# Kernel optimization log

Hardware: AMD Instinct MI355X
Metric: run time of the kernel (lower is better)

Reference implementation:

```python
import jax, jax.numpy as jnp
import numpy as np

H = 4096          # hidden_size (Llama-3.1-8B)
BLK = 32          # sca_block_size
NB = H // BLK     # 128 blocks
R = 4             # sca_block_rank
K = 3             # sca_top_k
SIGMA = 1.0       # sca_sigma
NUM_TASKS = 10


def setup_inputs() -> dict:
    key = jax.random.key(0)
    ks = jax.random.split(key, 9)
    B, S = 4, 4096
    x = jax.random.normal(ks[0], (B, S, H), jnp.float32)
    task_ids = jax.random.randint(ks[1], (B,), 0, NUM_TASKS)
    task_emb = jax.random.normal(ks[2], (NUM_TASKS, H), jnp.float32) * 0.02
    Wp = jax.random.normal(ks[3], (H, 3), jnp.float32) * (1.0 / np.sqrt(H))  # spatial_proj (xavier-ish)
    bp = jnp.zeros((3,), jnp.float32)
    centers = jax.random.normal(ks[4], (NB, 3), jnp.float32)                 # block_centers
    A = jax.random.normal(ks[5], (NB, H, R), jnp.float32) * 0.02             # per-block down proj
    Bm = jax.random.normal(ks[6], (NB, R, BLK), jnp.float32) * 0.02          # per-block up proj into its hidden slice
    adapter_scale = jnp.float32(1.0)
    return dict(x=x, task_ids=task_ids, task_emb=task_emb, Wp=Wp, bp=bp,
                centers=centers, A=A, Bm=Bm, adapter_scale=adapter_scale)


def reference(x, task_ids, task_emb, Wp, bp, centers, A, Bm, adapter_scale):
    # task conditioning
    h = x + task_emb[task_ids][:, None, :]                     # [B,S,H]
    # spatial routing: project tokens to 3D, Gaussian score vs block centers
    coords = h @ Wp + bp                                       # [B,S,3]
    d2 = jnp.sum((coords[:, :, None, :] - centers[None, None]) ** 2, axis=-1)  # [B,S,NB]
    scores = -d2 / (2.0 * SIGMA ** 2)
    top_s, top_i = jax.lax.top_k(scores, K)                    # [B,S,K]
    gates = jax.nn.softmax(top_s, axis=-1)                     # soft mask over selected blocks
    # low-rank adapter per block (dense spmm_impl): down-project against all blocks, gather top-k
    z = jnp.einsum('bsh,nhr->bsnr', h, A)                      # [B,S,NB,R]
    z_sel = jnp.take_along_axis(z, top_i[..., None], axis=2)   # [B,S,K,R]
    B_sel = Bm[top_i]                                          # [B,S,K,R,BLK]
    delta_blk = jnp.einsum('bskr,bskrc->bskc', z_sel, B_sel) * gates[..., None]  # [B,S,K,BLK]
    # scatter block outputs into their hidden slices
    Bn, Sn = x.shape[0], x.shape[1]
    cols = top_i[..., None] * BLK + jnp.arange(BLK)            # [B,S,K,BLK]
    bi = jnp.arange(Bn)[:, None, None, None]
    si = jnp.arange(Sn)[None, :, None, None]
    delta = jnp.zeros_like(x).at[bi, si, cols].add(delta_blk)  # [B,S,H]
    return x + adapter_scale * delta
```

## Files before the change

kernel.cpp:

```cpp
#include <hip/hip_runtime.h>
#include <math.h>

#define HDIM 4096
#define NBLK 128
#define RNK  4
#define TOPK 3

typedef float f4 __attribute__((ext_vector_type(4)));
typedef float f2 __attribute__((ext_vector_type(2)));
typedef unsigned int u32;
typedef u32 u4 __attribute__((ext_vector_type(4)));

__device__ __forceinline__ u32 pk_fp8(f4 v) {
    u32 w = (u32)__builtin_amdgcn_cvt_pk_fp8_f32(v.x, v.y, 0, false);
    w = (u32)__builtin_amdgcn_cvt_pk_fp8_f32(v.z, v.w, (int)w, true);
    return w;
}
__device__ __forceinline__ f2 upk_fp8(u32 w, bool hi) {
    typedef float vf2 __attribute__((ext_vector_type(2)));
    vf2 r = hi ? __builtin_amdgcn_cvt_pk_f32_fp8((int)w, true)
               : __builtin_amdgcn_cvt_pk_f32_fp8((int)w, false);
    f2 o; o.x = r.x; o.y = r.y; return o;
}

__global__ __launch_bounds__(256) void convert_A8(
    const float* __restrict__ A, u32* __restrict__ Af8)
{
    int d = blockIdx.x * 256 + threadIdx.x;
    const f4* src = reinterpret_cast<const f4*>(A) + 4 * (size_t)d;
    f4 r0 = __builtin_nontemporal_load(src + 0);
    f4 r1 = __builtin_nontemporal_load(src + 1);
    f4 r2 = __builtin_nontemporal_load(src + 2);
    f4 r3 = __builtin_nontemporal_load(src + 3);
    u4 o;
    o.x = pk_fp8(r0); o.y = pk_fp8(r1); o.z = pk_fp8(r2); o.w = pk_fp8(r3);
    reinterpret_cast<u4*>(Af8)[d] = o;
}

__global__ __launch_bounds__(256) void npl_fused(
    const float* __restrict__ x,
    const int*   __restrict__ task_ids,
    const float* __restrict__ task_emb,
    const float* __restrict__ Wp,
    const float* __restrict__ bp,
    const float* __restrict__ centers,
    const u32*   __restrict__ Af8,
    const float* __restrict__ Bm,
    const float* __restrict__ scale_p,
    float* __restrict__ out,
    int S_per_batch)
{
    __shared__ float h_lds[HDIM];
    __shared__ float redc[4][4];
    __shared__ float redz[4][12];

    const int tid  = threadIdx.x;
    const int wid  = tid >> 6;
    const int lane = tid & 63;
    const int token = blockIdx.x;
    const int b = token / S_per_batch;
    const int task = task_ids[b];

    const float* xrow = x + (size_t)token * HDIM;
    const float* trow = task_emb + (size_t)task * HDIM;
    float*       orow = out + (size_t)token * HDIM;

    const f4* xr4 = reinterpret_cast<const f4*>(xrow);
    const f4* tr4 = reinterpret_cast<const f4*>(trow);
    f4*       or4 = reinterpret_cast<f4*>(orow);

    f4 xv[4];
    float c0 = 0.f, c1 = 0.f, c2 = 0.f;
#pragma unroll
    for (int k = 0; k < 4; ++k) {
        int i4 = tid + k * 256;
        f4 xx = __builtin_nontemporal_load(xr4 + i4);
        f4 tt = tr4[i4];
        xv[k] = xx;
        f4 hh = xx + tt;
        reinterpret_cast<f4*>(h_lds)[i4] = hh;
        int e = i4 * 4;
        const float* wrow = Wp + (size_t)e * 3;
        c0 += hh.x * wrow[0];  c1 += hh.x * wrow[1];  c2 += hh.x * wrow[2];
        c0 += hh.y * wrow[3];  c1 += hh.y * wrow[4];  c2 += hh.y * wrow[5];
        c0 += hh.z * wrow[6];  c1 += hh.z * wrow[7];  c2 += hh.z * wrow[8];
        c0 += hh.w * wrow[9];  c1 += hh.w * wrow[10]; c2 += hh.w * wrow[11];
    }
#pragma unroll
    for (int off = 32; off; off >>= 1) {
        c0 += __shfl_down(c0, off);
        c1 += __shfl_down(c1, off);
        c2 += __shfl_down(c2, off);
    }
    if (lane == 0) { redc[wid][0] = c0; redc[wid][1] = c1; redc[wid][2] = c2; }
    __syncthreads();

    c0 = redc[0][0] + redc[1][0] + redc[2][0] + redc[3][0] + bp[0];
    c1 = redc[0][1] + redc[1][1] + redc[2][1] + redc[3][1] + bp[1];
    c2 = redc[0][2] + redc[1][2] + redc[2][2] + redc[3][2] + bp[2];

    float dx = c0 - centers[lane * 3 + 0];
    float dy = c1 - centers[lane * 3 + 1];
    float dz = c2 - centers[lane * 3 + 2];
    float v1 = -0.5f * (dx * dx + dy * dy + dz * dz);
    dx = c0 - centers[(lane + 64) * 3 + 0];
    dy = c1 - centers[(lane + 64) * 3 + 1];
    dz = c2 - centers[(lane + 64) * 3 + 2];
    float v2 = -0.5f * (dx * dx + dy * dy + dz * dz);

    float tv0, tv1, tv2; int n0, n1, n2;
#pragma unroll
    for (int kk = 0; kk < TOPK; ++kk) {
        float v = v1; int idx = lane;
        if (v2 > v || (v2 == v && (lane + 64) < idx)) { v = v2; idx = lane + 64; }
#pragma unroll
        for (int off = 32; off; off >>= 1) {
            float ov = __shfl_down(v, off);
            int   oi = __shfl_down(idx, off);
            if (ov > v || (ov == v && oi < idx)) { v = ov; idx = oi; }
        }
        idx = __shfl(idx, 0);
        v   = __shfl(v, 0);
        if (kk == 0)      { tv0 = v; n0 = idx; }
        else if (kk == 1) { tv1 = v; n1 = idx; }
        else              { tv2 = v; n2 = idx; }
        if (idx == lane)      v1 = -3.0e38f;
        if (idx == lane + 64) v2 = -3.0e38f;
    }

    float m  = tv0;
    float e0 = 1.0f;
    float e1 = expf(tv1 - m);
    float e2 = expf(tv2 - m);
    float inv = 1.0f / (e0 + e1 + e2);
    float s = scale_p[0];
    float g0 = e0 * inv * s;
    float g1 = e1 * inv * s;
    float g2 = e2 * inv * s;

    float zp[TOPK][RNK];
#pragma unroll
    for (int kk = 0; kk < TOPK; ++kk)
#pragma unroll
        for (int r = 0; r < RNK; ++r) zp[kk][r] = 0.f;

#pragma unroll
    for (int kk = 0; kk < TOPK; ++kk) {
        int n = (kk == 0) ? n0 : (kk == 1) ? n1 : n2;
        const u4* Ab = reinterpret_cast<const u4*>(Af8) + (size_t)n * 1024;
#pragma unroll
        for (int k = 0; k < 4; ++k) {
            int idx = tid + k * 256;
            u4 q = Ab[idx];
            f4 hv = reinterpret_cast<const f4*>(h_lds)[idx];
            f2 p;
            p = upk_fp8(q.x, false); zp[kk][0] += hv.x * p.x; zp[kk][1] += hv.x * p.y;
            p = upk_fp8(q.x, true);  zp[kk][2] += hv.x * p.x; zp[kk][3] += hv.x * p.y;
            p = upk_fp8(q.y, false); zp[kk][0] += hv.y * p.x; zp[kk][1] += hv.y * p.y;
            p = upk_fp8(q.y, true);  zp[kk][2] += hv.y * p.x; zp[kk][3] += hv.y * p.y;
            p = upk_fp8(q.z, false); zp[kk][0] += hv.z * p.x; zp[kk][1] += hv.z * p.y;
            p = upk_fp8(q.z, true);  zp[kk][2] += hv.z * p.x; zp[kk][3] += hv.z * p.y;
            p = upk_fp8(q.w, false); zp[kk][0] += hv.w * p.x; zp[kk][1] += hv.w * p.y;
            p = upk_fp8(q.w, true);  zp[kk][2] += hv.w * p.x; zp[kk][3] += hv.w * p.y;
        }
    }
#pragma unroll
    for (int off = 32; off; off >>= 1) {
#pragma unroll
        for (int kk = 0; kk < TOPK; ++kk)
#pragma unroll
            for (int r = 0; r < RNK; ++r)
                zp[kk][r] += __shfl_down(zp[kk][r], off);
    }
    if (lane == 0) {
#pragma unroll
        for (int kk = 0; kk < TOPK; ++kk)
#pragma unroll
            for (int r = 0; r < RNK; ++r)
                redz[wid][kk * RNK + r] = zp[kk][r];
    }
    __syncthreads();

    float zf_[12];
#pragma unroll
    for (int t = 0; t < 12; ++t)
        zf_[t] = redz[0][t] + redz[1][t] + redz[2][t] + redz[3][t];

#pragma unroll
    for (int k = 0; k < 4; ++k) {
        int i4 = tid + k * 256;
        int e = i4 * 4;
        int bb = e >> 5;
        f4 o = xv[k];
        int kk = (bb == n0) ? 0 : (bb == n1) ? 1 : (bb == n2) ? 2 : -1;
        if (kk >= 0) {
            int nn = (kk == 0) ? n0 : (kk == 1) ? n1 : n2;
            float za = (kk == 0) ? zf_[0] : (kk == 1) ? zf_[4] : zf_[8];
            float zb = (kk == 0) ? zf_[1] : (kk == 1) ? zf_[5] : zf_[9];
            float zc = (kk == 0) ? zf_[2] : (kk == 1) ? zf_[6] : zf_[10];
            float zd = (kk == 0) ? zf_[3] : (kk == 1) ? zf_[7] : zf_[11];
            float gg = (kk == 0) ? g0 : (kk == 1) ? g1 : g2;
            const float* bm = Bm + (size_t)nn * 128;
            int c = e & 31;
            float d0 = za * bm[c + 0] + zb * bm[32 + c + 0] + zc * bm[64 + c + 0] + zd * bm[96 + c + 0];
            float d1 = za * bm[c + 1] + zb * bm[32 + c + 1] + zc * bm[64 + c + 1] + zd * bm[96 + c + 1];
            float d2 = za * bm[c + 2] + zb * bm[32 + c + 2] + zc * bm[64 + c + 2] + zd * bm[96 + c + 2];
            float d3 = za * bm[c + 3] + zb * bm[32 + c + 3] + zc * bm[64 + c + 3] + zd * bm[96 + c + 3];
            o.x += d0 * gg;
            o.y += d1 * gg;
            o.z += d2 * gg;
            o.w += d3 * gg;
        }
        __builtin_nontemporal_store(o, or4 + i4);
    }
}

extern "C" void kernel_launch(void* const* d_in, const int* in_sizes, int n_in,
                              void* d_out, int out_size, void* d_ws, size_t ws_size,
                              hipStream_t stream) {
    const float* x        = (const float*)d_in[0];
    const int*   task_ids = (const int*)  d_in[1];
    const float* task_emb = (const float*)d_in[2];
    const float* Wp       = (const float*)d_in[3];
    const float* bp       = (const float*)d_in[4];
    const float* centers  = (const float*)d_in[5];
    const float* A        = (const float*)d_in[6];
    const float* Bm       = (const float*)d_in[7];
    const float* scale    = (const float*)d_in[8];

    int tokens = in_sizes[0] / HDIM;
    int B      = in_sizes[1];
    int S      = tokens / B;

    u32* Af8 = (u32*)d_ws;

    const int n_u4 = NBLK * HDIM * RNK / 16;
    convert_A8<<<dim3(n_u4 / 256), dim3(256), 0, stream>>>(A, Af8);
    npl_fused<<<dim3(tokens), dim3(256), 0, stream>>>(
        x, task_ids, task_emb, Wp, bp, centers, Af8, Bm, scale,
        (float*)d_out, S);
}
```

Measured before the change: 196.4 us.

## Single-pass top-3 wave merge, interleave A loads, drop cached x registers

Replaces the three serial argmax wave reductions with one butterfly pass that merges sorted top-3 lists across lanes. The fp8 A-row loads for the three selected blocks are interleaved so all three are in flight at once. x is no longer kept in registers; the output rebuilds it as h minus the task embedding reread from LDS and global memory. This lowers register pressure and latency at the cost of extra reads, and the subtraction may not reproduce x exactly in floating point.

```diff
diff --git a/kernel.cpp b/kernel.cpp
--- a/kernel.cpp
+++ b/kernel.cpp
@@ -69,14 +69,12 @@
     const f4* tr4 = reinterpret_cast<const f4*>(trow);
     f4*       or4 = reinterpret_cast<f4*>(orow);
 
-    f4 xv[4];
     float c0 = 0.f, c1 = 0.f, c2 = 0.f;
 #pragma unroll
     for (int k = 0; k < 4; ++k) {
         int i4 = tid + k * 256;
         f4 xx = __builtin_nontemporal_load(xr4 + i4);
         f4 tt = tr4[i4];
-        xv[k] = xx;
         f4 hh = xx + tt;
         reinterpret_cast<f4*>(h_lds)[i4] = hh;
         int e = i4 * 4;
@@ -108,25 +106,34 @@
     dz = c2 - centers[(lane + 64) * 3 + 2];
     float v2 = -0.5f * (dx * dx + dy * dy + dz * dz);
 
-    float tv0, tv1, tv2; int n0, n1, n2;
-#pragma unroll
-    for (int kk = 0; kk < TOPK; ++kk) {
-        float v = v1; int idx = lane;
-        if (v2 > v || (v2 == v && (lane + 64) < idx)) { v = v2; idx = lane + 64; }
-#pragma unroll
-        for (int off = 32; off; off >>= 1) {
-            float ov = __shfl_down(v, off);
-            int   oi = __shfl_down(idx, off);
-            if (ov > v || (ov == v && oi < idx)) { v = ov; idx = oi; }
-        }
-        idx = __shfl(idx, 0);
-        v   = __shfl(v, 0);
-        if (kk == 0)      { tv0 = v; n0 = idx; }
-        else if (kk == 1) { tv1 = v; n1 = idx; }
-        else              { tv2 = v; n2 = idx; }
-        if (idx == lane)      v1 = -3.0e38f;
-        if (idx == lane + 64) v2 = -3.0e38f;
-    }
+    float av, bv, cv; int ai, bi, ci;
+    {
+        bool f = (v1 > v2) || (v1 == v2);
+        av = f ? v1 : v2;  ai = f ? lane : (lane + 64);
+        bv = f ? v2 : v1;  bi = f ? (lane + 64) : lane;
+        cv = -3.0e38f;     ci = 0x7fffffff;
+    }
+#pragma unroll
+    for (int off = 1; off < 64; off <<= 1) {
+        float oav = __shfl_xor(av, off); int oai = __shfl_xor(ai, off);
+        float obv = __shfl_xor(bv, off); int obi = __shfl_xor(bi, off);
+        float ocv = __shfl_xor(cv, off); int oci = __shfl_xor(ci, off);
+        bool t0 = (av > oav) || (av == oav && ai < oai);
+        float r0v = t0 ? av : oav;  int r0i = t0 ? ai : oai;
+        float lhv = t0 ? bv : av;   int lhi = t0 ? bi : ai;
+        float lnv = t0 ? cv : bv;   int lni = t0 ? ci : bi;
+        float mhv = t0 ? oav : obv; int mhi = t0 ? oai : obi;
+        float mnv = t0 ? obv : ocv; int mni = t0 ? obi : oci;
+        bool t1 = (lhv > mhv) || (lhv == mhv && lhi < mhi);
+        float r1v = t1 ? lhv : mhv; int r1i = t1 ? lhi : mhi;
+        float l2v = t1 ? lnv : lhv; int l2i = t1 ? lni : lhi;
+        float m2v = t1 ? mhv : mnv; int m2i = t1 ? mhi : mni;
+        bool t2 = (l2v > m2v) || (l2v == m2v && l2i < m2i);
+        float r2v = t2 ? l2v : m2v; int r2i = t2 ? l2i : m2i;
+        av = r0v; ai = r0i; bv = r1v; bi = r1i; cv = r2v; ci = r2i;
+    }
+    float tv0 = av, tv1 = bv, tv2 = cv;
+    int   n0  = ai, n1  = bi, n2  = ci;
 
     float m  = tv0;
     float e0 = 1.0f;
@@ -144,24 +151,44 @@
 #pragma unroll
         for (int r = 0; r < RNK; ++r) zp[kk][r] = 0.f;
 
-#pragma unroll
-    for (int kk = 0; kk < TOPK; ++kk) {
-        int n = (kk == 0) ? n0 : (kk == 1) ? n1 : n2;
-        const u4* Ab = reinterpret_cast<const u4*>(Af8) + (size_t)n * 1024;
+    {
+        const u4* A0 = reinterpret_cast<const u4*>(Af8) + (size_t)n0 * 1024;
+        const u4* A1 = reinterpret_cast<const u4*>(Af8) + (size_t)n1 * 1024;
+        const u4* A2 = reinterpret_cast<const u4*>(Af8) + (size_t)n2 * 1024;
 #pragma unroll
         for (int k = 0; k < 4; ++k) {
             int idx = tid + k * 256;
-            u4 q = Ab[idx];
+            u4 q0 = A0[idx];
+            u4 q1 = A1[idx];
+            u4 q2 = A2[idx];
             f4 hv = reinterpret_cast<const f4*>(h_lds)[idx];
             f2 p;
-            p = upk_fp8(q.x, false); zp[kk][0] += hv.x * p.x; zp[kk][1] += hv.x * p.y;
-            p = upk_fp8(q.x, true);  zp[kk][2] += hv.x * p.x; zp[kk][3] += hv.x * p.y;
-            p = upk_fp8(q.y, false); zp[kk][0] += hv.y * p.x; zp[kk][1] += hv.y * p.y;
-            p = upk_fp8(q.y, true);  zp[kk][2] += hv.y * p.x; zp[kk][3] += hv.y * p.y;
-            p = upk_fp8(q.z, false); zp[kk][0] += hv.z * p.x; zp[kk][1] += hv.z * p.y;
-            p = upk_fp8(q.z, true);  zp[kk][2] += hv.z * p.x; zp[kk][3] += hv.z * p.y;
-            p = upk_fp8(q.w, false); zp[kk][0] += hv.w * p.x; zp[kk][1] += hv.w * p.y;
-            p = upk_fp8(q.w, true);  zp[kk][2] += hv.w * p.x; zp[kk][3] += hv.w * p.y;
+            p = upk_fp8(q0.x, false); zp[0][0] += hv.x * p.x; zp[0][1] += hv.x * p.y;
+            p = upk_fp8(q0.x, true);  zp[0][2] += hv.x * p.x; zp[0][3] += hv.x * p.y;
+            p = upk_fp8(q0.y, false); zp[0][0] += hv.y * p.x; zp[0][1] += hv.y * p.y;
+            p = upk_fp8(q0.y, true);  zp[0][2] += hv.y * p.x; zp[0][3] += hv.y * p.y;
+            p = upk_fp8(q0.z, false); zp[0][0] += hv.z * p.x; zp[0][1] += hv.z * p.y;
+            p = upk_fp8(q0.z, true);  zp[0][2] += hv.z * p.x; zp[0][3] += hv.z * p.y;
+            p = upk_fp8(q0.w, false); zp[0][0] += hv.w * p.x; zp[0][1] += hv.w * p.y;
+            p = upk_fp8(q0.w, true);  zp[0][2] += hv.w * p.x; zp[0][3] += hv.w * p.y;
+
+            p = upk_fp8(q1.x, false); zp[1][0] += hv.x * p.x; zp[1][1] += hv.x * p.y;
+            p = upk_fp8(q1.x, true);  zp[1][2] += hv.x * p.x; zp[1][3] += hv.x * p.y;
+            p = upk_fp8(q1.y, false); zp[1][0] += hv.y * p.x; zp[1][1] += hv.y * p.y;
+            p = upk_fp8(q1.y, true);  zp[1][2] += hv.y * p.x; zp[1][3] += hv.y * p.y;
+            p = upk_fp8(q1.z, false); zp[1][0] += hv.z * p.x; zp[1][1] += hv.z * p.y;
+            p = upk_fp8(q1.z, true);  zp[1][2] += hv.z * p.x; zp[1][3] += hv.z * p.y;
+            p = upk_fp8(q1.w, false); zp[1][0] += hv.w * p.x; zp[1][1] += hv.w * p.y;
+            p = upk_fp8(q1.w, true);  zp[1][2] += hv.w * p.x; zp[1][3] += hv.w * p.y;
+
+            p = upk_fp8(q2.x, false); zp[2][0] += hv.x * p.x; zp[2][1] += hv.x * p.y;
+            p = upk_fp8(q2.x, true);  zp[2][2] += hv.x * p.x; zp[2][3] += hv.x * p.y;
+            p = upk_fp8(q2.y, false); zp[2][0] += hv.y * p.x; zp[2][1] += hv.y * p.y;
+            p = upk_fp8(q2.y, true);  zp[2][2] += hv.y * p.x; zp[2][3] += hv.y * p.y;
+            p = upk_fp8(q2.z, false); zp[2][0] += hv.z * p.x; zp[2][1] += hv.z * p.y;
+            p = upk_fp8(q2.z, true);  zp[2][2] += hv.z * p.x; zp[2][3] += hv.z * p.y;
+            p = upk_fp8(q2.w, false); zp[2][0] += hv.w * p.x; zp[2][1] += hv.w * p.y;
+            p = upk_fp8(q2.w, true);  zp[2][2] += hv.w * p.x; zp[2][3] += hv.w * p.y;
         }
     }
 #pragma unroll
@@ -191,7 +218,9 @@
         int i4 = tid + k * 256;
         int e = i4 * 4;
         int bb = e >> 5;
-        f4 o = xv[k];
+        f4 hh = reinterpret_cast<const f4*>(h_lds)[i4];
+        f4 tt = tr4[i4];
+        f4 o = hh - tt;
         int kk = (bb == n0) ? 0 : (bb == n1) ? 1 : (bb == n2) ? 2 : -1;
         if (kk >= 0) {
             int nn = (kk == 0) ? n0 : (kk == 1) ? n1 : n2;
```

New measurement: 204.0 us. 3.9% more time.

## Process two tokens per block with fp16 LDS and a single-pass top-3 merge

Applied to the files above, without the earlier changes.

Each 256-thread block now handles two tokens, launching half as many blocks. The task-conditioned hidden row is stored in LDS as packed fp16 instead of fp32, so both rows fit. The output residual is rebuilt as h minus task_emb rather than keeping x in registers. The three sequential top-1 reductions are replaced by one butterfly merge of per-lane top-3 lists, and the three A-block loads are interleaved. The aim is to cut barriers, register pressure and routing latency per token and to keep more memory traffic in flight. The cost is fp16 rounding error on the residual x path and on h in the down-projection, plus the extra task_emb reread.

```diff
diff --git a/kernel.cpp b/kernel.cpp
--- a/kernel.cpp
+++ b/kernel.cpp
@@ -8,6 +8,7 @@
 
 typedef float f4 __attribute__((ext_vector_type(4)));
 typedef float f2 __attribute__((ext_vector_type(2)));
+typedef _Float16 h2 __attribute__((ext_vector_type(2)));
 typedef unsigned int u32;
 typedef u32 u4 __attribute__((ext_vector_type(4)));
 
@@ -21,6 +22,10 @@
     vf2 r = hi ? __builtin_amdgcn_cvt_pk_f32_fp8((int)w, true)
                : __builtin_amdgcn_cvt_pk_f32_fp8((int)w, false);
     f2 o; o.x = r.x; o.y = r.y; return o;
+}
+__device__ __forceinline__ u32 pk_f16(float a, float b) {
+    h2 r; r.x = (_Float16)a; r.y = (_Float16)b;
+    return __builtin_bit_cast(u32, r);
 }
 
 __global__ __launch_bounds__(256) void convert_A8(
@@ -50,35 +55,35 @@
     float* __restrict__ out,
     int S_per_batch)
 {
-    __shared__ float h_lds[HDIM];
-    __shared__ float redc[4][4];
-    __shared__ float redz[4][12];
+    __shared__ u32  h_pk[2][HDIM / 2];
+    __shared__ float redc[2][4][4];
+    __shared__ float redz[2][4][12];
 
     const int tid  = threadIdx.x;
     const int wid  = tid >> 6;
     const int lane = tid & 63;
-    const int token = blockIdx.x;
-    const int b = token / S_per_batch;
-    const int task = task_ids[b];
-
-    const float* xrow = x + (size_t)token * HDIM;
-    const float* trow = task_emb + (size_t)task * HDIM;
-    float*       orow = out + (size_t)token * HDIM;
-
-    const f4* xr4 = reinterpret_cast<const f4*>(xrow);
-    const f4* tr4 = reinterpret_cast<const f4*>(trow);
-    f4*       or4 = reinterpret_cast<f4*>(orow);
-
-    f4 xv[4];
+    const int t0   = blockIdx.x * 2;
+    const int t1   = t0 + 1;
+
+    const int b0 = t0 / S_per_batch, b1 = t1 / S_per_batch;
+    const int task0 = task_ids[b0], task1 = task_ids[b1];
+
+    const f4* xr0 = reinterpret_cast<const f4*>(x + (size_t)t0 * HDIM);
+    const f4* xr1 = reinterpret_cast<const f4*>(x + (size_t)t1 * HDIM);
+    const f4* tr0 = reinterpret_cast<const f4*>(task_emb + (size_t)task0 * HDIM);
+    const f4* tr1 = reinterpret_cast<const f4*>(task_emb + (size_t)task1 * HDIM);
+    f4* or0 = reinterpret_cast<f4*>(out + (size_t)t0 * HDIM);
+    f4* or1 = reinterpret_cast<f4*>(out + (size_t)t1 * HDIM);
+
     float c0 = 0.f, c1 = 0.f, c2 = 0.f;
 #pragma unroll
     for (int k = 0; k < 4; ++k) {
         int i4 = tid + k * 256;
-        f4 xx = __builtin_nontemporal_load(xr4 + i4);
-        f4 tt = tr4[i4];
-        xv[k] = xx;
+        f4 xx = __builtin_nontemporal_load(xr0 + i4);
+        f4 tt = tr0[i4];
         f4 hh = xx + tt;
-        reinterpret_cast<f4*>(h_lds)[i4] = hh;
+        h_pk[0][2 * i4]     = pk_f16(hh.x, hh.y);
+        h_pk[0][2 * i4 + 1] = pk_f16(hh.z, hh.w);
         int e = i4 * 4;
         const float* wrow = Wp + (size_t)e * 3;
         c0 += hh.x * wrow[0];  c1 += hh.x * wrow[1];  c2 += hh.x * wrow[2];
@@ -92,127 +97,199 @@
         c1 += __shfl_down(c1, off);
         c2 += __shfl_down(c2, off);
     }
-    if (lane == 0) { redc[wid][0] = c0; redc[wid][1] = c1; redc[wid][2] = c2; }
-    __syncthreads();
-
-    c0 = redc[0][0] + redc[1][0] + redc[2][0] + redc[3][0] + bp[0];
-    c1 = redc[0][1] + redc[1][1] + redc[2][1] + redc[3][1] + bp[1];
-    c2 = redc[0][2] + redc[1][2] + redc[2][2] + redc[3][2] + bp[2];
-
-    float dx = c0 - centers[lane * 3 + 0];
-    float dy = c1 - centers[lane * 3 + 1];
-    float dz = c2 - centers[lane * 3 + 2];
-    float v1 = -0.5f * (dx * dx + dy * dy + dz * dz);
-    dx = c0 - centers[(lane + 64) * 3 + 0];
-    dy = c1 - centers[(lane + 64) * 3 + 1];
-    dz = c2 - centers[(lane + 64) * 3 + 2];
-    float v2 = -0.5f * (dx * dx + dy * dy + dz * dz);
-
-    float tv0, tv1, tv2; int n0, n1, n2;
-#pragma unroll
-    for (int kk = 0; kk < TOPK; ++kk) {
-        float v = v1; int idx = lane;
-        if (v2 > v || (v2 == v && (lane + 64) < idx)) { v = v2; idx = lane + 64; }
-#pragma unroll
-        for (int off = 32; off; off >>= 1) {
-            float ov = __shfl_down(v, off);
-            int   oi = __shfl_down(idx, off);
-            if (ov > v || (ov == v && oi < idx)) { v = ov; idx = oi; }
-        }
-        idx = __shfl(idx, 0);
-        v   = __shfl(v, 0);
-        if (kk == 0)      { tv0 = v; n0 = idx; }
-        else if (kk == 1) { tv1 = v; n1 = idx; }
-        else              { tv2 = v; n2 = idx; }
-        if (idx == lane)      v1 = -3.0e38f;
-        if (idx == lane + 64) v2 = -3.0e38f;
-    }
-
-    float m  = tv0;
-    float e0 = 1.0f;
-    float e1 = expf(tv1 - m);
-    float e2 = expf(tv2 - m);
-    float inv = 1.0f / (e0 + e1 + e2);
-    float s = scale_p[0];
-    float g0 = e0 * inv * s;
-    float g1 = e1 * inv * s;
-    float g2 = e2 * inv * s;
-
-    float zp[TOPK][RNK];
-#pragma unroll
-    for (int kk = 0; kk < TOPK; ++kk)
-#pragma unroll
-        for (int r = 0; r < RNK; ++r) zp[kk][r] = 0.f;
-
-#pragma unroll
-    for (int kk = 0; kk < TOPK; ++kk) {
-        int n = (kk == 0) ? n0 : (kk == 1) ? n1 : n2;
-        const u4* Ab = reinterpret_cast<const u4*>(Af8) + (size_t)n * 1024;
-#pragma unroll
-        for (int k = 0; k < 4; ++k) {
-            int idx = tid + k * 256;
-            u4 q = Ab[idx];
-            f4 hv = reinterpret_cast<const f4*>(h_lds)[idx];
-            f2 p;
-            p = upk_fp8(q.x, false); zp[kk][0] += hv.x * p.x; zp[kk][1] += hv.x * p.y;
-            p = upk_fp8(q.x, true);  zp[kk][2] += hv.x * p.x; zp[kk][3] += hv.x * p.y;
-            p = upk_fp8(q.y, false); zp[kk][0] += hv.y * p.x; zp[kk][1] += hv.y * p.y;
-            p = upk_fp8(q.y, true);  zp[kk][2] += hv.y * p.x; zp[kk][3] += hv.y * p.y;
-            p = upk_fp8(q.z, false); zp[kk][0] += hv.z * p.x; zp[kk][1] += hv.z * p.y;
-            p = upk_fp8(q.z, true);  zp[kk][2] += hv.z * p.x; zp[kk][3] += hv.z * p.y;
-            p = upk_fp8(q.w, false); zp[kk][0] += hv.w * p.x; zp[kk][1] += hv.w * p.y;
-            p = upk_fp8(q.w, true);  zp[kk][2] += hv.w * p.x; zp[kk][3] += hv.w * p.y;
-        }
-    }
-#pragma unroll
-    for (int off = 32; off; off >>= 1) {
-#pragma unroll
-        for (int kk = 0; kk < TOPK; ++kk)
-#pragma unroll
-            for (int r = 0; r < RNK; ++r)
-                zp[kk][r] += __shfl_down(zp[kk][r], off);
-    }
-    if (lane == 0) {
-#pragma unroll
-        for (int kk = 0; kk < TOPK; ++kk)
-#pragma unroll
-            for (int r = 0; r < RNK; ++r)
-                redz[wid][kk * RNK + r] = zp[kk][r];
-    }
-    __syncthreads();
-
-    float zf_[12];
-#pragma unroll
-    for (int t = 0; t < 12; ++t)
-        zf_[t] = redz[0][t] + redz[1][t] + redz[2][t] + redz[3][t];
-
+    if (lane == 0) { redc[0][wid][0] = c0; redc[0][wid][1] = c1; redc[0][wid][2] = c2; }
+
+    c0 = 0.f; c1 = 0.f; c2 = 0.f;
 #pragma unroll
     for (int k = 0; k < 4; ++k) {
         int i4 = tid + k * 256;
+        f4 xx = __builtin_nontemporal_load(xr1 + i4);
+        f4 tt = tr1[i4];
+        f4 hh = xx + tt;
+        h_pk[1][2 * i4]     = pk_f16(hh.x, hh.y);
+        h_pk[1][2 * i4 + 1] = pk_f16(hh.z, hh.w);
         int e = i4 * 4;
-        int bb = e >> 5;
-        f4 o = xv[k];
-        int kk = (bb == n0) ? 0 : (bb == n1) ? 1 : (bb == n2) ? 2 : -1;
-        if (kk >= 0) {
-            int nn = (kk == 0) ? n0 : (kk == 1) ? n1 : n2;
-            float za = (kk == 0) ? zf_[0] : (kk == 1) ? zf_[4] : zf_[8];
-            float zb = (kk == 0) ? zf_[1] : (kk == 1) ? zf_[5] : zf_[9];
-            float zc = (kk == 0) ? zf_[2] : (kk == 1) ? zf_[6] : zf_[10];
-            float zd = (kk == 0) ? zf_[3] : (kk == 1) ? zf_[7] : zf_[11];
-            float gg = (kk == 0) ? g0 : (kk == 1) ? g1 : g2;
-            const float* bm = Bm + (size_t)nn * 128;
-            int c = e & 31;
-            float d0 = za * bm[c + 0] + zb * bm[32 + c + 0] + zc * bm[64 + c + 0] + zd * bm[96 + c + 0];
-            float d1 = za * bm[c + 1] + zb * bm[32 + c + 1] + zc * bm[64 + c + 1] + zd * bm[96 + c + 1];
-            float d2 = za * bm[c + 2] + zb * bm[32 + c + 2] + zc * bm[64 + c + 2] + zd * bm[96 + c + 2];
-            float d3 = za * bm[c + 3] + zb * bm[32 + c + 3] + zc * bm[64 + c + 3] + zd * bm[96 + c + 3];
-            o.x += d0 * gg;
-            o.y += d1 * gg;
-            o.z += d2 * gg;
-            o.w += d3 * gg;
-        }
-        __builtin_nontemporal_store(o, or4 + i4);
-    }
+        const float* wrow = Wp + (size_t)e * 3;
+        c0 += hh.x * wrow[0];  c1 += hh.x * wrow[1];  c2 += hh.x * wrow[2];
+        c0 += hh.y * wrow[3];  c1 += hh.y * wrow[4];  c2 += hh.y * wrow[5];
+        c0 += hh.z * wrow[6];  c1 += hh.z * wrow[7];  c2 += hh.z * wrow[8];
+        c0 += hh.w * wrow[9];  c1 += hh.w * wrow[10]; c2 += hh.w * wrow[11];
+    }
+#pragma unroll
+    for (int off = 32; off; off >>= 1) {
+        c0 += __shfl_down(c0, off);
+        c1 += __shfl_down(c1, off);
+        c2 += __shfl_down(c2, off);
+    }
+    if (lane == 0) { redc[1][wid][0] = c0; redc[1][wid][1] = c1; redc[1][wid][2] = c2; }
+
+    __syncthreads();
+
+    int n0a, n1a, n2a; float g0a, g1a, g2a;
+    int n0b, n1b, n2b; float g0b, g1b, g2b;
+    const float sgl = scale_p[0];
+
+#define ROUTE_AND_Z(T, N0, N1, N2, G0, G1, G2)                                    \
+    {                                                                             \
+        float cc0 = redc[T][0][0] + redc[T][1][0] + redc[T][2][0] + redc[T][3][0] + bp[0]; \
+        float cc1 = redc[T][0][1] + redc[T][1][1] + redc[T][2][1] + redc[T][3][1] + bp[1]; \
+        float cc2 = redc[T][0][2] + redc[T][1][2] + redc[T][2][2] + redc[T][3][2] + bp[2]; \
+        float dx = cc0 - centers[lane * 3 + 0];                                   \
+        float dy = cc1 - centers[lane * 3 + 1];                                   \
+        float dz = cc2 - centers[lane * 3 + 2];                                   \
+        float v1 = -0.5f * (dx * dx + dy * dy + dz * dz);                         \
+        dx = cc0 - centers[(lane + 64) * 3 + 0];                                  \
+        dy = cc1 - centers[(lane + 64) * 3 + 1];                                  \
+        dz = cc2 - centers[(lane + 64) * 3 + 2];                                  \
+        float v2 = -0.5f * (dx * dx + dy * dy + dz * dz);                         \
+        float av, bv, cv; int ai, bi, ci;                                         \
+        {                                                                         \
+            bool f = (v1 > v2) || (v1 == v2);                                     \
+            av = f ? v1 : v2;  ai = f ? lane : (lane + 64);                       \
+            bv = f ? v2 : v1;  bi = f ? (lane + 64) : lane;                       \
+            cv = -3.0e38f;     ci = 0x7fffffff;                                   \
+        }                                                                         \
+        _Pragma("unroll")                                                         \
+        for (int off = 1; off < 64; off <<= 1) {                                  \
+            float oav = __shfl_xor(av, off); int oai = __shfl_xor(ai, off);       \
+            float obv = __shfl_xor(bv, off); int obi = __shfl_xor(bi, off);       \
+            float ocv = __shfl_xor(cv, off); int oci = __shfl_xor(ci, off);       \
+            bool u0 = (av > oav) || (av == oav && ai < oai);                      \
+            float r0v = u0 ? av : oav;  int r0i = u0 ? ai : oai;                  \
+            float lhv = u0 ? bv : av;   int lhi = u0 ? bi : ai;                   \
+            float lnv = u0 ? cv : bv;   int lni = u0 ? ci : bi;                   \
+            float mhv = u0 ? oav : obv; int mhi = u0 ? oai : obi;                 \
+            float mnv = u0 ? obv : ocv; int mni = u0 ? obi : oci;                 \
+            bool u1 = (lhv > mhv) || (lhv == mhv && lhi < mhi);                   \
+            float r1v = u1 ? lhv : mhv; int r1i = u1 ? lhi : mhi;                 \
+            float l2v = u1 ? lnv : lhv; int l2i = u1 ? lni : lhi;                 \
+            float m2v = u1 ? mhv : mnv; int m2i = u1 ? mhi : mni;                 \
+            bool u2 = (l2v > m2v) || (l2v == m2v && l2i < m2i);                   \
+            float r2v = u2 ? l2v : m2v; int r2i = u2 ? l2i : m2i;                 \
+            av = r0v; ai = r0i; bv = r1v; bi = r1i; cv = r2v; ci = r2i;           \
+        }                                                                         \
+        N0 = ai; N1 = bi; N2 = ci;                                                \
+        float e1g = expf(bv - av);                                                \
+        float e2g = expf(cv - av);                                                \
+        float invg = 1.0f / (1.0f + e1g + e2g);                                   \
+        G0 = 1.0f * invg * sgl;                                                   \
+        G1 = e1g * invg * sgl;                                                    \
+        G2 = e2g * invg * sgl;                                                    \
+        float zp0[RNK] = {0.f, 0.f, 0.f, 0.f};                                    \
+        float zp1[RNK] = {0.f, 0.f, 0.f, 0.f};                                    \
+        float zp2[RNK] = {0.f, 0.f, 0.f, 0.f};                                    \
+        const u4* A0 = reinterpret_cast<const u4*>(Af8) + (size_t)N0 * 1024;      \
+        const u4* A1 = reinterpret_cast<const u4*>(Af8) + (size_t)N1 * 1024;      \
+        const u4* A2 = reinterpret_cast<const u4*>(Af8) + (size_t)N2 * 1024;      \
+        _Pragma("unroll")                                                         \
+        for (int k = 0; k < 4; ++k) {                                             \
+            int idx = tid + k * 256;                                              \
+            u4 q0 = A0[idx];                                                      \
+            u4 q1 = A1[idx];                                                      \
+            u4 q2 = A2[idx];                                                      \
+            u32 pa = h_pk[T][2 * idx], pb = h_pk[T][2 * idx + 1];                 \
+            h2 ha2 = __builtin_bit_cast(h2, pa);                                  \
+            h2 hb2 = __builtin_bit_cast(h2, pb);                                  \
+            float hx = (float)ha2.x, hy = (float)ha2.y;                           \
+            float hz = (float)hb2.x, hw = (float)hb2.y;                           \
+            f2 p;                                                                 \
+            p = upk_fp8(q0.x, false); zp0[0] += hx * p.x; zp0[1] += hx * p.y;     \
+            p = upk_fp8(q0.x, true);  zp0[2] += hx * p.x; zp0[3] += hx * p.y;     \
+            p = upk_fp8(q0.y, false); zp0[0] += hy * p.x; zp0[1] += hy * p.y;     \
+            p = upk_fp8(q0.y, true);  zp0[2] += hy * p.x; zp0[3] += hy * p.y;     \
+            p = upk_fp8(q0.z, false); zp0[0] += hz * p.x; zp0[1] += hz * p.y;     \
+            p = upk_fp8(q0.z, true);  zp0[2] += hz * p.x; zp0[3] += hz * p.y;     \
+            p = upk_fp8(q0.w, false); zp0[0] += hw * p.x; zp0[1] += hw * p.y;     \
+            p = upk_fp8(q0.w, true);  zp0[2] += hw * p.x; zp0[3] += hw * p.y;     \
+            p = upk_fp8(q1.x, false); zp1[0] += hx * p.x; zp1[1] += hx * p.y;     \
+            p = upk_fp8(q1.x, true);  zp1[2] += hx * p.x; zp1[3] += hx * p.y;     \
+            p = upk_fp8(q1.y, false); zp1[0] += hy * p.x; zp1[1] += hy * p.y;     \
+            p = upk_fp8(q1.y, true);  zp1[2] += hy * p.x; zp1[3] += hy * p.y;     \
+            p = upk_fp8(q1.z, false); zp1[0] += hz * p.x; zp1[1] += hz * p.y;     \
+            p = upk_fp8(q1.z, true);  zp1[2] += hz * p.x; zp1[3] += hz * p.y;     \
+            p = upk_fp8(q1.w, false); zp1[0] += hw * p.x; zp1[1] += hw * p.y;     \
+            p = upk_fp8(q1.w, true);  zp1[2] += hw * p.x; zp1[3] += hw * p.y;     \
+            p = upk_fp8(q2.x, false); zp2[0] += hx * p.x; zp2[1] += hx * p.y;     \
+            p = upk_fp8(q2.x, true);  zp2[2] += hx * p.x; zp2[3] += hx * p.y;     \
+            p = upk_fp8(q2.y, false); zp2[0] += hy * p.x; zp2[1] += hy * p.y;     \
+            p = upk_fp8(q2.y, true);  zp2[2] += hy * p.x; zp2[3] += hy * p.y;     \
+            p = upk_fp8(q2.z, false); zp2[0] += hz * p.x; zp2[1] += hz * p.y;     \
+            p = upk_fp8(q2.z, true);  zp2[2] += hz * p.x; zp2[3] += hz * p.y;     \
+            p = upk_fp8(q2.w, false); zp2[0] += hw * p.x; zp2[1] += hw * p.y;     \
+            p = upk_fp8(q2.w, true);  zp2[2] += hw * p.x; zp2[3] += hw * p.y;     \
+        }                                                                         \
+        _Pragma("unroll")                                                         \
+        for (int off = 32; off; off >>= 1) {                                      \
+            _Pragma("unroll")                                                     \
+            for (int r = 0; r < RNK; ++r) {                                       \
+                zp0[r] += __shfl_down(zp0[r], off);                               \
+                zp1[r] += __shfl_down(zp1[r], off);                               \
+                zp2[r] += __shfl_down(zp2[r], off);                               \
+            }                                                                     \
+        }                                                                         \
+        if (lane == 0) {                                                          \
+            _Pragma("unroll")                                                     \
+            for (int r = 0; r < RNK; ++r) {                                       \
+                redz[T][wid][0 * RNK + r] = zp0[r];                               \
+                redz[T][wid][1 * RNK + r] = zp1[r];                               \
+                redz[T][wid][2 * RNK + r] = zp2[r];                               \
+            }                                                                     \
+        }                                                                         \
+    }
+
+    ROUTE_AND_Z(0, n0a, n1a, n2a, g0a, g1a, g2a)
+    ROUTE_AND_Z(1, n0b, n1b, n2b, g0b, g1b, g2b)
+
+    __syncthreads();
+
+#define OUT_PHASE(T, TR, OR, N0, N1, N2, G0, G1, G2)                              \
+    {                                                                             \
+        float zf_[12];                                                            \
+        _Pragma("unroll")                                                         \
+        for (int t = 0; t < 12; ++t)                                              \
+            zf_[t] = redz[T][0][t] + redz[T][1][t] + redz[T][2][t] + redz[T][3][t]; \
+        _Pragma("unroll")                                                         \
+        for (int k = 0; k < 4; ++k) {                                             \
+            int i4 = tid + k * 256;                                               \
+            int e = i4 * 4;                                                       \
+            int bb = e >> 5;                                                      \
+            u32 pa = h_pk[T][2 * i4], pb = h_pk[T][2 * i4 + 1];                   \
+            h2 ha2 = __builtin_bit_cast(h2, pa);                                  \
+            h2 hb2 = __builtin_bit_cast(h2, pb);                                  \
+            f4 tt = TR[i4];                                                       \
+            f4 o;                                                                 \
+            o.x = (float)ha2.x - tt.x;                                            \
+            o.y = (float)ha2.y - tt.y;                                            \
+            o.z = (float)hb2.x - tt.z;                                            \
+            o.w = (float)hb2.y - tt.w;                                            \
+            int kk = (bb == N0) ? 0 : (bb == N1) ? 1 : (bb == N2) ? 2 : -1;       \
+            if (kk >= 0) {                                                        \
+                int nn = (kk == 0) ? N0 : (kk == 1) ? N1 : N2;                    \
+                float za = (kk == 0) ? zf_[0] : (kk == 1) ? zf_[4] : zf_[8];      \
+                float zb = (kk == 0) ? zf_[1] : (kk == 1) ? zf_[5] : zf_[9];      \
+                float zc = (kk == 0) ? zf_[2] : (kk == 1) ? zf_[6] : zf_[10];     \
+                float zd = (kk == 0) ? zf_[3] : (kk == 1) ? zf_[7] : zf_[11];     \
+                float gg = (kk == 0) ? G0 : (kk == 1) ? G1 : G2;                  \
+                const float* bm = Bm + (size_t)nn * 128;                          \
+                int c = e & 31;                                                   \
+                float d0 = za * bm[c + 0] + zb * bm[32 + c + 0] + zc * bm[64 + c + 0] + zd * bm[96 + c + 0]; \
+                float d1 = za * bm[c + 1] + zb * bm[32 + c + 1] + zc * bm[64 + c + 1] + zd * bm[96 + c + 1]; \
+                float d2 = za * bm[c + 2] + zb * bm[32 + c + 2] + zc * bm[64 + c + 2] + zd * bm[96 + c + 2]; \
+                float d3 = za * bm[c + 3] + zb * bm[32 + c + 3] + zc * bm[64 + c + 3] + zd * bm[96 + c + 3]; \
+                o.x += d0 * gg;                                                   \
+                o.y += d1 * gg;                                                   \
+                o.z += d2 * gg;                                                   \
+                o.w += d3 * gg;                                                   \
+            }                                                                     \
+            __builtin_nontemporal_store(o, OR + i4);                              \
+        }                                                                         \
+    }
+
+    OUT_PHASE(0, tr0, or0, n0a, n1a, n2a, g0a, g1a, g2a)
+    OUT_PHASE(1, tr1, or1, n0b, n1b, n2b, g0b, g1b, g2b)
+
+#undef ROUTE_AND_Z
+#undef OUT_PHASE
 }
 
 extern "C" void kernel_launch(void* const* d_in, const int* in_sizes, int n_in,
@@ -236,7 +313,7 @@
 
     const int n_u4 = NBLK * HDIM * RNK / 16;
     convert_A8<<<dim3(n_u4 / 256), dim3(256), 0, stream>>>(A, Af8);
-    npl_fused<<<dim3(tokens), dim3(256), 0, stream>>>(
+    npl_fused<<<dim3(tokens / 2), dim3(256), 0, stream>>>(
         x, task_ids, task_emb, Wp, bp, centers, Af8, Bm, scale,
         (float*)d_out, S);
 }
```

Result: slower. 248.5 us (+26.5%).
